# Optimization experiments

Hardware: AMD Instinct MI355X
Metric: run time of the kernel (lower is better)

The kernel has to match this reference:

```python
import jax, jax.numpy as jnp
import numpy as np

N_NODES = 100000
N_EDGES = 1600000
FEAT = 128
HID = 128
CLASSES = 10
GRAPHS = 64


def gcn_conv(x, W, b, src, dst, n):
    # PyG GCNConv: h = x @ W; add self-loops; symmetric deg^{-1/2} norm; scatter-add; + bias
    h = x @ W
    src_f = jnp.concatenate([src, jnp.arange(n, dtype=src.dtype)])
    dst_f = jnp.concatenate([dst, jnp.arange(n, dtype=dst.dtype)])
    deg = jax.ops.segment_sum(jnp.ones_like(dst_f, dtype=h.dtype), dst_f, num_segments=n)
    dinv = jax.lax.rsqrt(jnp.where(deg > 0, deg, 1.0))
    norm = dinv[src_f] * dinv[dst_f]              # [E+N]
    msg = h[src_f] * norm[:, None]                # gather + scale
    out = jax.ops.segment_sum(msg, dst_f, num_segments=n)  # scatter-add
    return out + b


def global_mean_pool(x, batch, num_graphs):
    s = jax.ops.segment_sum(x, batch, num_segments=num_graphs)
    cnt = jax.ops.segment_sum(jnp.ones_like(batch, dtype=x.dtype), batch, num_segments=num_graphs)
    return s / jnp.maximum(cnt, 1.0)[:, None]


def setup_inputs() -> dict:
    key = jax.random.key(0)
    ks = jax.random.split(key, 10)
    x = jax.random.normal(ks[0], (N_NODES, FEAT), dtype=jnp.float32)
    edge_index = jax.random.randint(ks[1], (2, N_EDGES), 0, N_NODES, dtype=jnp.int64)
    batch = jnp.sort(jax.random.randint(ks[2], (N_NODES,), 0, GRAPHS, dtype=jnp.int64))
    def glorot(k, fi, fo):
        s = float(np.sqrt(6.0 / (fi + fo)))
        return jax.random.uniform(k, (fi, fo), jnp.float32, -s, s)
    return {
        "x": x, "edge_index": edge_index, "batch": batch,
        "W1": glorot(ks[3], FEAT, HID), "b1": jnp.zeros((HID,), jnp.float32),
        "W2": glorot(ks[4], HID, HID), "b2": jnp.zeros((HID,), jnp.float32),
        "W3": glorot(ks[5], HID, HID), "b3": jnp.zeros((HID,), jnp.float32),
        "Wlin": glorot(ks[6], HID, CLASSES), "blin": jnp.zeros((CLASSES,), jnp.float32),
    }


def reference(x, edge_index, batch, W1, b1, W2, b2, W3, b3, Wlin, blin):
    src, dst = edge_index[0], edge_index[1]
    n = x.shape[0]
    h = jax.nn.relu(gcn_conv(x, W1, b1, src, dst, n))
    h = jax.nn.relu(gcn_conv(h, W2, b2, src, dst, n))
    h = gcn_conv(h, W3, b3, src, dst, n)
    emb = global_mean_pool(h, batch, GRAPHS)      # [GRAPHS, HID]
    # dropout(p=0.5) is identity in eval mode
    logits = emb @ Wlin + blin                    # [GRAPHS, CLASSES]
    return logits, jnp.squeeze(emb)
```

## Files before the change

kernel.cpp:

```cpp
#include <hip/hip_runtime.h>
#include <hip/hip_bf16.h>
#include <stdint.h>

typedef unsigned int uint32;
typedef __attribute__((ext_vector_type(8))) short short8;
typedef __attribute__((ext_vector_type(4))) float float4v;

#define FEAT 128
#define NGRAPH 64
#define GB   256
#define NBK  512

__device__ __forceinline__ float bf2f_lo(uint32 v) {
    union { uint32 i; float f; } u; u.i = v << 16; return u.f;
}
__device__ __forceinline__ float bf2f_hi(uint32 v) {
    union { uint32 i; float f; } u; u.i = v & 0xffff0000u; return u.f;
}
__device__ __forceinline__ unsigned short f2bf(float f) {
    uint32 u = __builtin_bit_cast(uint32, f);
    uint32 r = (u + 0x7fffu + ((u >> 16) & 1u)) >> 16;
    return (unsigned short)r;
}
__device__ __forceinline__ uint32 f2bf2(float lo, float hi) {
    return (uint32)f2bf(lo) | ((uint32)f2bf(hi) << 16);
}

__global__ void k_bhist(const int* __restrict__ dst, int* __restrict__ bhistT,
                        float* __restrict__ pool, int* __restrict__ cntg, int E) {
    __shared__ int h[NBK];
    int t = threadIdx.x, blk = blockIdx.x;
    if (blk == 0) {
        for (int i = t; i < NGRAPH * FEAT; i += 256) pool[i] = 0.f;
        if (t < NGRAPH) cntg[t] = 0;
    }
    for (int b = t; b < NBK; b += 256) h[b] = 0;
    __syncthreads();
    int chunk = (E + GB - 1) / GB;
    int lo = blk * chunk, hi = min(lo + chunk, E);
    for (int e = lo + t; e < hi; e += 256)
        atomicAdd(&h[dst[e] >> 8], 1);
    __syncthreads();
    for (int b = t; b < NBK; b += 256) bhistT[b * GB + blk] = h[b];
}

__global__ void k_boffs_a(int* __restrict__ bhistT, int* __restrict__ btot) {
    int b = blockIdx.x, l = threadIdx.x;
    int v[4];
    int base = b * GB + l * 4;
#pragma unroll
    for (int j = 0; j < 4; j++) v[j] = bhistT[base + j];
    int s = v[0] + v[1] + v[2] + v[3];
    int incl = s;
    for (int off = 1; off < 64; off <<= 1) {
        int u = __shfl_up(incl, off);
        if (l >= off) incl += u;
    }
    int excl = incl - s;
    int p0 = excl, p1 = p0 + v[0], p2 = p1 + v[1], p3 = p2 + v[2];
    bhistT[base + 0] = p0; bhistT[base + 1] = p1;
    bhistT[base + 2] = p2; bhistT[base + 3] = p3;
    if (l == 63) btot[b] = incl;
}

__global__ void k_boffs_b(const int* __restrict__ btot, int* __restrict__ bbase) {
    __shared__ int sc[NBK];
    int t = threadIdx.x;
    int s = btot[t];
    sc[t] = s;
    __syncthreads();
    for (int off = 1; off < NBK; off <<= 1) {
        int v = (t >= off) ? sc[t - off] : 0;
        __syncthreads();
        sc[t] += v;
        __syncthreads();
    }
    bbase[t] = sc[t] - s;
    if (t == NBK - 1) bbase[NBK] = sc[t];
}

__global__ void k_bscat(const int* __restrict__ src, const int* __restrict__ dst,
                        const int* __restrict__ bhistT, const int* __restrict__ bbase,
                        uint32* __restrict__ ebuf, int E) {
    __shared__ int cur[NBK];
    int t = threadIdx.x, blk = blockIdx.x;
    for (int b = t; b < NBK; b += 256) cur[b] = bbase[b] + bhistT[b * GB + blk];
    __syncthreads();
    int chunk = (E + GB - 1) / GB;
    int lo = blk * chunk, hi = min(lo + chunk, E);
    for (int e = lo + t; e < hi; e += 256) {
        int d = dst[e], s = src[e];
        int b = d >> 8;
        int p = atomicAdd(&cur[b], 1);
        ebuf[p] = ((uint32)s << 8) | (uint32)(d & 255);
    }
}

__global__ void k_csr(const uint32* __restrict__ ebuf, const int* __restrict__ bbase,
                      float* __restrict__ dinv, int* __restrict__ rowp,
                      int* __restrict__ csrc, int N, int E) {
    __shared__ int h[256];
    __shared__ int cur[256];
    int t = threadIdx.x, b = blockIdx.x;
    h[t] = 0;
    __syncthreads();
    int e0 = bbase[b], e1 = bbase[b + 1];
    for (int e = e0 + t; e < e1; e += 256)
        atomicAdd(&h[ebuf[e] & 255u], 1);
    __syncthreads();
    int deg = h[t];
    cur[t] = deg;
    __syncthreads();
    for (int off = 1; off < 256; off <<= 1) {
        int v = (t >= off) ? cur[t - off] : 0;
        __syncthreads();
        cur[t] += v;
        __syncthreads();
    }
    int r = bbase[b] + cur[t] - deg;
    int node = b * 256 + t;
    if (node < N) {
        rowp[node] = r;
        dinv[node] = rsqrtf((float)deg + 1.0f);
    }
    if (b == 0 && t == 0) rowp[N] = E;
    cur[t] = r;
    __syncthreads();
    for (int e = e0 + t; e < e1; e += 256) {
        uint32 v = ebuf[e];
        int p = atomicAdd(&cur[v & 255u], 1);
        csrc[p] = (int)(v >> 8);
    }
}

__global__ void k_wswz3(const float* __restrict__ W1, const float* __restrict__ W2,
                        const float* __restrict__ W3, unsigned short* __restrict__ o1,
                        unsigned short* __restrict__ o2, unsigned short* __restrict__ o3) {
    int wid = blockIdx.x >> 3;
    const float* W = (wid == 0) ? W1 : (wid == 1) ? W2 : W3;
    unsigned short* out = (wid == 0) ? o1 : (wid == 1) ? o2 : o3;
    int e = (blockIdx.x & 7) * 256 + threadIdx.x;
    int kt = e >> 9, ct = (e >> 6) & 7, lane = e & 63;
    int krow = kt * 32 + (lane >> 4) * 8;
    int col = ct * 16 + (lane & 15);
#pragma unroll
    for (int j = 0; j < 8; j++)
        out[e * 8 + j] = f2bf(W[(krow + j) * FEAT + col]);
}

template <bool F32IN>
__global__ void k_gemm(const void* __restrict__ Xp,
                       const unsigned short* __restrict__ Wswz,
                       const float* __restrict__ dinv,
                       unsigned short* __restrict__ Hb, int N) {
    __shared__ unsigned short Wl[FEAT * FEAT];
    {
        const uint4* Wg = (const uint4*)Wswz;
        uint4* Ws = (uint4*)Wl;
        for (int i = threadIdx.x; i < 2048; i += 256) Ws[i] = Wg[i];
    }
    __syncthreads();

    int wave = threadIdx.x >> 6, lane = threadIdx.x & 63;
    int r0 = (blockIdx.x * 4 + wave) * 16;
    if (r0 >= N) return;
    int m = lane & 15, q = lane >> 4;

    int arow = r0 + m; if (arow >= N) arow = N - 1;
    short8 a[4];
    if (F32IN) {
        const float* Ar = (const float*)Xp + (long)arow * FEAT;
#pragma unroll
        for (int kt = 0; kt < 4; kt++) {
            float4 u = *(const float4*)(Ar + kt * 32 + q * 8);
            float4 v = *(const float4*)(Ar + kt * 32 + q * 8 + 4);
            short8 tv;
            tv[0] = (short)f2bf(u.x); tv[1] = (short)f2bf(u.y);
            tv[2] = (short)f2bf(u.z); tv[3] = (short)f2bf(u.w);
            tv[4] = (short)f2bf(v.x); tv[5] = (short)f2bf(v.y);
            tv[6] = (short)f2bf(v.z); tv[7] = (short)f2bf(v.w);
            a[kt] = tv;
        }
    } else {
        const short8* Ar = (const short8*)((const unsigned short*)Xp + (long)arow * FEAT);
#pragma unroll
        for (int kt = 0; kt < 4; kt++) a[kt] = Ar[kt * 4 + q];
    }

    const short8* Bl = (const short8*)Wl;
    float4v acc[8];
#pragma unroll
    for (int ct = 0; ct < 8; ct++) acc[ct] = (float4v){0.f, 0.f, 0.f, 0.f};
#pragma unroll
    for (int ct = 0; ct < 8; ct++) {
        acc[ct] = __builtin_amdgcn_mfma_f32_16x16x32_bf16(Bl[(0 * 8 + ct) * 64 + lane], a[0], acc[ct], 0, 0, 0);
        acc[ct] = __builtin_amdgcn_mfma_f32_16x16x32_bf16(Bl[(1 * 8 + ct) * 64 + lane], a[1], acc[ct], 0, 0, 0);
        acc[ct] = __builtin_amdgcn_mfma_f32_16x16x32_bf16(Bl[(2 * 8 + ct) * 64 + lane], a[2], acc[ct], 0, 0, 0);
        acc[ct] = __builtin_amdgcn_mfma_f32_16x16x32_bf16(Bl[(3 * 8 + ct) * 64 + lane], a[3], acc[ct], 0, 0, 0);
    }

    int node = r0 + m;
    bool ok = (node < N);
    float d = ok ? dinv[node] : 0.f;
#pragma unroll
    for (int ct = 0; ct < 8; ct++) {
        if (ok) {
            uint2 o;
            o.x = f2bf2(acc[ct][0] * d, acc[ct][1] * d);
            o.y = f2bf2(acc[ct][2] * d, acc[ct][3] * d);
            ((uint2*)(Hb + (long)node * FEAT + ct * 16))[q] = o;
        }
    }
}

__global__ void k_agg(const uint32* __restrict__ Hb,
                      const int* __restrict__ rowp, const int* __restrict__ csrc,
                      const float* __restrict__ dinv, const float* __restrict__ bias,
                      uint32* __restrict__ OUTb, int N, int relu) {
    int wave = threadIdx.x >> 6, lane = threadIdx.x & 63;
    int i = blockIdx.x * 4 + wave;
    if (i >= N) return;
    int f = lane & 31, half = lane >> 5;
    const uint2* H2 = (const uint2*)Hb;
    float a0 = 0.f, a1 = 0.f, a2 = 0.f, a3 = 0.f;
    int e0 = rowp[i], e1 = rowp[i + 1];
    int e = e0;
    for (; e + 16 <= e1; e += 16) {
        int  s[8];
        uint2 h[8];
#pragma unroll
        for (int j = 0; j < 8; j++) s[j] = csrc[e + 2 * j + half];
#pragma unroll
        for (int j = 0; j < 8; j++) h[j] = H2[(long)s[j] * 32 + f];
#pragma unroll
        for (int j = 0; j < 8; j++) {
            a0 += bf2f_lo(h[j].x); a1 += bf2f_hi(h[j].x);
            a2 += bf2f_lo(h[j].y); a3 += bf2f_hi(h[j].y);
        }
    }
    {
        int r = e1 - e;
        int  s[8];
        uint2 h[8];
#pragma unroll
        for (int j = 0; j < 8; j++) {
            int idx = 2 * j + half;
            if (idx < r) s[j] = csrc[e + idx];
        }
#pragma unroll
        for (int j = 0; j < 8; j++)
            if (2 * j + half < r) h[j] = H2[(long)s[j] * 32 + f];
#pragma unroll
        for (int j = 0; j < 8; j++)
            if (2 * j + half < r) {
                a0 += bf2f_lo(h[j].x); a1 += bf2f_hi(h[j].x);
                a2 += bf2f_lo(h[j].y); a3 += bf2f_hi(h[j].y);
            }
    }
    a0 += __shfl_xor(a0, 32);
    a1 += __shfl_xor(a1, 32);
    a2 += __shfl_xor(a2, 32);
    a3 += __shfl_xor(a3, 32);
    if (half == 0) {
        uint2 hv = H2[(long)i * 32 + f];
        a0 += bf2f_lo(hv.x); a1 += bf2f_hi(hv.x);
        a2 += bf2f_lo(hv.y); a3 += bf2f_hi(hv.y);
        float di = dinv[i];
        float4 bb = ((const float4*)bias)[f];
        a0 = a0 * di + bb.x; a1 = a1 * di + bb.y;
        a2 = a2 * di + bb.z; a3 = a3 * di + bb.w;
        if (relu) {
            a0 = fmaxf(a0, 0.f); a1 = fmaxf(a1, 0.f);
            a2 = fmaxf(a2, 0.f); a3 = fmaxf(a3, 0.f);
        }
        uint2 o;
        o.x = f2bf2(a0, a1);
        o.y = f2bf2(a2, a3);
        ((uint2*)OUTb)[(long)i * 32 + f] = o;
    }
}

__global__ void k_pool(const uint32* __restrict__ Gb, const int* __restrict__ batch,
                       float* __restrict__ pool, int* __restrict__ cntg, int N) {
    int t = threadIdx.x;
    int nb = gridDim.x;
    int chunk = (N + nb - 1) / nb;
    int lo = blockIdx.x * chunk, hi = min(lo + chunk, N);
    if (lo >= hi) return;
    float ax = 0.f, ay = 0.f;
    int cnt = 0;
    int cg = batch[lo];
    for (int i = lo; i < hi; i++) {
        int g = batch[i];
        if (g != cg) {
            atomicAdd(&pool[cg * FEAT + 2 * t], ax);
            atomicAdd(&pool[cg * FEAT + 2 * t + 1], ay);
            if (t == 0) atomicAdd(&cntg[cg], cnt);
            ax = ay = 0.f; cnt = 0; cg = g;
        }
        uint32 v = Gb[(long)i * 64 + t];
        ax += bf2f_lo(v); ay += bf2f_hi(v);
        cnt++;
    }
    atomicAdd(&pool[cg * FEAT + 2 * t], ax);
    atomicAdd(&pool[cg * FEAT + 2 * t + 1], ay);
    if (t == 0) atomicAdd(&cntg[cg], cnt);
}

__global__ void k_final(const float* __restrict__ pool, const int* __restrict__ cntg,
                        const float* __restrict__ Wlin, const float* __restrict__ blin,
                        float* __restrict__ out) {
    __shared__ float es[FEAT];
    int g = blockIdx.x, t = threadIdx.x;
    float c = (float)max(cntg[g], 1);
    float e = pool[g * FEAT + t] / c;
    es[t] = e;
    out[NGRAPH * 10 + g * FEAT + t] = e;
    __syncthreads();
    if (t < 10) {
        float a = blin[t];
        for (int k = 0; k < FEAT; k++)
            a += es[k] * Wlin[k * 10 + t];
        out[g * 10 + t] = a;
    }
}

extern "C" void kernel_launch(void* const* d_in, const int* in_sizes, int n_in,
                              void* d_out, int out_size, void* d_ws, size_t ws_size,
                              hipStream_t stream) {
    const float* x    = (const float*)d_in[0];
    const int*   ei   = (const int*)d_in[1];
    const int*   batch= (const int*)d_in[2];
    const float* W1   = (const float*)d_in[3];
    const float* b1   = (const float*)d_in[4];
    const float* W2   = (const float*)d_in[5];
    const float* b2   = (const float*)d_in[6];
    const float* W3   = (const float*)d_in[7];
    const float* b3   = (const float*)d_in[8];
    const float* Wlin = (const float*)d_in[9];
    const float* blin = (const float*)d_in[10];

    const int N = in_sizes[2];
    const int E = in_sizes[1] / 2;
    const int* src = ei;
    const int* dst = ei + E;
    const int NB = (N + 255) >> 8;

    char* w = (char*)d_ws;
    auto take = [&](size_t bytes) {
        char* p = w;
        w += (bytes + 255) & ~(size_t)255;
        return p;
    };
    float*  dinv   = (float*) take((size_t)N * 4);
    int*    rowp   = (int*)   take((size_t)(N + 1) * 4);
    int*    csrc   = (int*)   take((size_t)E * 4);
    uint32* ebuf   = (uint32*)take((size_t)E * 4);
    int*    bhistT = (int*)   take((size_t)GB * NBK * 4);
    int*    btot   = (int*)   take((size_t)NBK * 4);
    int*    bbase  = (int*)   take((size_t)(NBK + 1) * 4);
    uint32* hbuf   = (uint32*)take((size_t)N * FEAT * 2);
    uint32* gbuf   = (uint32*)take((size_t)N * FEAT * 2);
    unsigned short* w1s = (unsigned short*)take(FEAT * FEAT * 2);
    unsigned short* w2s = (unsigned short*)take(FEAT * FEAT * 2);
    unsigned short* w3s = (unsigned short*)take(FEAT * FEAT * 2);
    float*  pool   = (float*) take((size_t)NGRAPH * FEAT * 4);
    int*    cntg   = (int*)   take((size_t)NGRAPH * 4);
    (void)ws_size; (void)n_in; (void)out_size;

    k_bhist  <<<GB, 256, 0, stream>>>(dst, bhistT, pool, cntg, E);
    k_boffs_a<<<NBK, 64, 0, stream>>>(bhistT, btot);
    k_boffs_b<<<1, NBK, 0, stream>>>(btot, bbase);
    k_bscat  <<<GB, 256, 0, stream>>>(src, dst, bhistT, bbase, ebuf, E);
    k_csr    <<<NB, 256, 0, stream>>>(ebuf, bbase, dinv, rowp, csrc, N, E);

    k_wswz3<<<24, 256, 0, stream>>>(W1, W2, W3, w1s, w2s, w3s);

    const int tile_blocks = (N + 63) / 64;
    const int agg_blocks  = (N + 3) / 4;

    k_gemm<true> <<<tile_blocks, 256, 0, stream>>>(x, w1s, dinv, (unsigned short*)hbuf, N);
    k_agg<<<agg_blocks, 256, 0, stream>>>(hbuf, rowp, csrc, dinv, b1, gbuf, N, 1);
    k_gemm<false><<<tile_blocks, 256, 0, stream>>>(gbuf, w2s, dinv, (unsigned short*)hbuf, N);
    k_agg<<<agg_blocks, 256, 0, stream>>>(hbuf, rowp, csrc, dinv, b2, gbuf, N, 1);
    k_gemm<false><<<tile_blocks, 256, 0, stream>>>(gbuf, w3s, dinv, (unsigned short*)hbuf, N);
    k_agg<<<agg_blocks, 256, 0, stream>>>(hbuf, rowp, csrc, dinv, b3, gbuf, N, 0);

    k_pool <<<4096, 64, 0, stream>>>(gbuf, batch, pool, cntg, N);
    k_final<<<NGRAPH, 128, 0, stream>>>(pool, cntg, Wlin, blin, (float*)d_out);
}
```

Measured before the change: 429.4 us.

## Split aggregation feature dimension into quarter slices across interleaved blocks

The aggregation kernel now has each wave handle only a 32-feature quarter of a node's row. Lanes gather 4-byte words instead of 8-byte words, and four edge groups per wave are reduced with two shuffles. Blocks are interleaved so that consecutive block indices cover different quarters of neighbouring nodes, which aims to improve L2 locality of the gathered rows and to raise memory-level parallelism. In exchange the CSR indices are read four times, there are four times as many waves, and the gathers are narrower.

```diff
diff --git a/kernel.cpp b/kernel.cpp
--- a/kernel.cpp
+++ b/kernel.cpp
@@ -218,65 +218,52 @@
                       const float* __restrict__ dinv, const float* __restrict__ bias,
                       uint32* __restrict__ OUTb, int N, int relu) {
     int wave = threadIdx.x >> 6, lane = threadIdx.x & 63;
-    int i = blockIdx.x * 4 + wave;
+    int slot = blockIdx.x & 7;
+    int q = slot >> 1, s = slot & 1;
+    int i = ((blockIdx.x >> 3) * 2 + s) * 4 + wave;
     if (i >= N) return;
-    int f = lane & 31, half = lane >> 5;
-    const uint2* H2 = (const uint2*)Hb;
-    float a0 = 0.f, a1 = 0.f, a2 = 0.f, a3 = 0.f;
+    int u = lane & 15, qi = lane >> 4;
+    int qoff = q * 16;
+    float a0 = 0.f, a1 = 0.f;
     int e0 = rowp[i], e1 = rowp[i + 1];
     int e = e0;
-    for (; e + 16 <= e1; e += 16) {
-        int  s[8];
-        uint2 h[8];
-#pragma unroll
-        for (int j = 0; j < 8; j++) s[j] = csrc[e + 2 * j + half];
-#pragma unroll
-        for (int j = 0; j < 8; j++) h[j] = H2[(long)s[j] * 32 + f];
-#pragma unroll
-        for (int j = 0; j < 8; j++) {
-            a0 += bf2f_lo(h[j].x); a1 += bf2f_hi(h[j].x);
-            a2 += bf2f_lo(h[j].y); a3 += bf2f_hi(h[j].y);
-        }
+    for (; e + 32 <= e1; e += 32) {
+        int sx[8];
+        uint32 h[8];
+#pragma unroll
+        for (int j = 0; j < 8; j++) sx[j] = csrc[e + 4 * j + qi];
+#pragma unroll
+        for (int j = 0; j < 8; j++) h[j] = Hb[(long)sx[j] * 64 + qoff + u];
+#pragma unroll
+        for (int j = 0; j < 8; j++) { a0 += bf2f_lo(h[j]); a1 += bf2f_hi(h[j]); }
     }
     {
         int r = e1 - e;
-        int  s[8];
-        uint2 h[8];
+        int sx[8];
+        uint32 h[8];
 #pragma unroll
         for (int j = 0; j < 8; j++) {
-            int idx = 2 * j + half;
-            if (idx < r) s[j] = csrc[e + idx];
+            int idx = 4 * j + qi;
+            if (idx < r) sx[j] = csrc[e + idx];
         }
 #pragma unroll
         for (int j = 0; j < 8; j++)
-            if (2 * j + half < r) h[j] = H2[(long)s[j] * 32 + f];
+            if (4 * j + qi < r) h[j] = Hb[(long)sx[j] * 64 + qoff + u];
 #pragma unroll
         for (int j = 0; j < 8; j++)
-            if (2 * j + half < r) {
-                a0 += bf2f_lo(h[j].x); a1 += bf2f_hi(h[j].x);
-                a2 += bf2f_lo(h[j].y); a3 += bf2f_hi(h[j].y);
-            }
-    }
-    a0 += __shfl_xor(a0, 32);
-    a1 += __shfl_xor(a1, 32);
-    a2 += __shfl_xor(a2, 32);
-    a3 += __shfl_xor(a3, 32);
-    if (half == 0) {
-        uint2 hv = H2[(long)i * 32 + f];
-        a0 += bf2f_lo(hv.x); a1 += bf2f_hi(hv.x);
-        a2 += bf2f_lo(hv.y); a3 += bf2f_hi(hv.y);
+            if (4 * j + qi < r) { a0 += bf2f_lo(h[j]); a1 += bf2f_hi(h[j]); }
+    }
+    a0 += __shfl_xor(a0, 16); a1 += __shfl_xor(a1, 16);
+    a0 += __shfl_xor(a0, 32); a1 += __shfl_xor(a1, 32);
+    if (qi == 0) {
+        uint32 hv = Hb[(long)i * 64 + qoff + u];
+        a0 += bf2f_lo(hv); a1 += bf2f_hi(hv);
         float di = dinv[i];
-        float4 bb = ((const float4*)bias)[f];
-        a0 = a0 * di + bb.x; a1 = a1 * di + bb.y;
-        a2 = a2 * di + bb.z; a3 = a3 * di + bb.w;
-        if (relu) {
-            a0 = fmaxf(a0, 0.f); a1 = fmaxf(a1, 0.f);
-            a2 = fmaxf(a2, 0.f); a3 = fmaxf(a3, 0.f);
-        }
-        uint2 o;
-        o.x = f2bf2(a0, a1);
-        o.y = f2bf2(a2, a3);
-        ((uint2*)OUTb)[(long)i * 32 + f] = o;
+        float2 bb = ((const float2*)bias)[qoff + u];
+        a0 = a0 * di + bb.x;
+        a1 = a1 * di + bb.y;
+        if (relu) { a0 = fmaxf(a0, 0.f); a1 = fmaxf(a1, 0.f); }
+        OUTb[(long)i * 64 + qoff + u] = f2bf2(a0, a1);
     }
 }
 
@@ -377,7 +364,7 @@
     k_wswz3<<<24, 256, 0, stream>>>(W1, W2, W3, w1s, w2s, w3s);
 
     const int tile_blocks = (N + 63) / 64;
-    const int agg_blocks  = (N + 3) / 4;
+    const int agg_blocks  = ((N + 7) / 8) * 8;
 
     k_gemm<true> <<<tile_blocks, 256, 0, stream>>>(x, w1s, dinv, (unsigned short*)hbuf, N);
     k_agg<<<agg_blocks, 256, 0, stream>>>(hbuf, rowp, csrc, dinv, b1, gbuf, N, 1);
```

After: 758.9 us. 76.7% more time.
